# Kernel optimization log

Hardware: AMD Instinct MI355X
Metric: run time of the kernel (lower is better)

## Reference

```python
import jax, jax.numpy as jnp
import numpy as np

B, S, D, H = 2, 2048, 1024, 16  # batch, seq, rep_dim, num_heads
DH = D // H
MASK_VALUE = -1e-06  # value passed by MHAttention to masked_softmax (NOT -1e6)


def setup_inputs() -> dict:
    key = jax.random.key(0)
    ks = jax.random.split(key, 16)
    def xavier(k, shape):
        fan_in, fan_out = shape[0], shape[1]
        limit = float(np.sqrt(6.0 / (fan_in + fan_out)))
        return jax.random.uniform(k, shape, jnp.float32, -limit, limit)
    return {
        "queries": jax.random.normal(ks[0], (B, S, D), jnp.float32),
        "keys": jax.random.normal(ks[1], (B, S, D), jnp.float32),
        "values": jax.random.normal(ks[2], (B, S, D), jnp.float32),
        "thresholds": jax.random.randint(ks[3], (B,), 1, S + 1, jnp.int32),
        # Linear params stored as (in, out) so y = x @ W + b
        "Wq": xavier(ks[4], (D, D)), "bq": jnp.zeros((D,), jnp.float32),
        "Wk": xavier(ks[5], (D, D)), "bk": jnp.zeros((D,), jnp.float32),
        "Wv": xavier(ks[6], (D, D)), "bv": jnp.zeros((D,), jnp.float32),
        "W": xavier(ks[7], (DH, DH)),  # learnable bilinear attention matrix
        "Wo": xavier(ks[8], (D, D)), "bo": jnp.zeros((D,), jnp.float32),
    }


def reference(queries, keys, values, thresholds, Wq, bq, Wk, bk, Wv, bv, W, Wo, bo):
    def split_heads(x):  # (B,S,D) -> (B,H,S,DH)
        return x.reshape(B, S, H, DH).transpose(0, 2, 1, 3)

    Q = split_heads(queries @ Wq + bq)
    K = split_heads(keys @ Wk + bk)
    V = split_heads(values @ Wv + bv)

    # bilinear scores: (Q @ W) @ K^T, no 1/sqrt(d) scaling in original
    scores = jnp.einsum("bhqd,bhkd->bhqk", Q @ W, K)
    # mask key positions >= threshold[b] with MASK_VALUE before softmax
    keep = jnp.arange(S)[None, None, None, :] < thresholds[:, None, None, None]
    scores = jnp.where(keep, scores, MASK_VALUE)
    attn = jax.nn.softmax(scores, axis=-1)

    out = jnp.einsum("bhqk,bhkd->bhqd", attn, V)
    out = out.transpose(0, 2, 1, 3).reshape(B, S, D)  # merge heads
    return out @ Wo + bo
```

## Files before the change

### kernel.cpp

```cpp
#include <hip/hip_runtime.h>
#include <hip/hip_bf16.h>

#define D_MODEL 1024
#define NHEADS  16
#define DH      64
#define SEQ     2048
#define BATCH   2

#define LOG2E 1.4426950408889634f
#define MASKB2 (-1e-6f * LOG2E)
#define DEFER_THR 11.5456f
#define NEG_INF (-__builtin_inff())

typedef __attribute__((ext_vector_type(8))) short short8;
typedef __attribute__((ext_vector_type(4))) short short4v;
typedef __attribute__((ext_vector_type(4))) float f32x4;

#define AS1C(p) ((const __attribute__((address_space(1))) void*)(p))
#define AS3(p)  ((__attribute__((address_space(3))) void*)(p))

union PB { short4v s4; unsigned int u[2]; };

static __device__ __forceinline__ float fexp2(float x) {
    return __builtin_amdgcn_exp2f(x);
}

static __device__ __forceinline__ unsigned int pk2(float lo, float hi) {
    __hip_bfloat16 a = __float2bfloat16(lo), b = __float2bfloat16(hi);
    unsigned short au = *(unsigned short*)&a, bu = *(unsigned short*)&b;
    return (unsigned int)au | ((unsigned int)bu << 16);
}

__global__ __launch_bounds__(256) void fold_kernel(const float* __restrict__ Wq,
                                                   const float* __restrict__ bq,
                                                   const float* __restrict__ W,
                                                   float* __restrict__ Wq2,
                                                   float* __restrict__ bq2) {
    if (blockIdx.x < 4096) {
        int idx = blockIdx.x * 256 + threadIdx.x;
        int row = idx >> 10;
        int col = idx & 1023;
        int h = col >> 6, j = col & 63;
        const float* wqr = Wq + (size_t)row * D_MODEL + h * DH;
        float s = 0.f;
#pragma unroll
        for (int d = 0; d < DH; ++d) s += wqr[d] * W[d * DH + j];
        Wq2[idx] = s * LOG2E;
    } else {
        int col = (blockIdx.x - 4096) * 256 + threadIdx.x;
        int h = col >> 6, j = col & 63;
        float s = 0.f;
#pragma unroll
        for (int d = 0; d < DH; ++d) s += bq[h * DH + d] * W[d * DH + j];
        bq2[col] = s * LOG2E;
    }
}

__global__ __launch_bounds__(256) void convert3_kernel(const float* __restrict__ q,
                                                       const float* __restrict__ k,
                                                       const float* __restrict__ v,
                                                       __hip_bfloat16* __restrict__ oq,
                                                       __hip_bfloat16* __restrict__ ok,
                                                       __hip_bfloat16* __restrict__ ov) {
    int z = blockIdx.x >> 11;
    int i = (blockIdx.x & 2047) * 256 + threadIdx.x;
    const float* in = (z == 0) ? q : (z == 1) ? k : v;
    __hip_bfloat16* out = (z == 0) ? oq : (z == 1) ? ok : ov;
    float4 a = *(const float4*)(in + (size_t)i * 8);
    float4 b = *(const float4*)(in + (size_t)i * 8 + 4);
    __hip_bfloat16 o[8];
    o[0] = __float2bfloat16(a.x); o[1] = __float2bfloat16(a.y);
    o[2] = __float2bfloat16(a.z); o[3] = __float2bfloat16(a.w);
    o[4] = __float2bfloat16(b.x); o[5] = __float2bfloat16(b.y);
    o[6] = __float2bfloat16(b.z); o[7] = __float2bfloat16(b.w);
    *(short8*)(out + (size_t)i * 8) = *(short8*)o;
}

__global__ __launch_bounds__(256) void transpose4_kernel(const float* __restrict__ W0,
                                                         const float* __restrict__ W1,
                                                         const float* __restrict__ W2,
                                                         const float* __restrict__ W3,
                                                         __hip_bfloat16* __restrict__ T0,
                                                         __hip_bfloat16* __restrict__ T1,
                                                         __hip_bfloat16* __restrict__ T2,
                                                         __hip_bfloat16* __restrict__ T3) {
    __shared__ float sT[32][33];
    int z = blockIdx.z;
    const float* Win = (z == 0) ? W0 : (z == 1) ? W1 : (z == 2) ? W2 : W3;
    __hip_bfloat16* Wt = (z == 0) ? T0 : (z == 1) ? T1 : (z == 2) ? T2 : T3;
    int n0 = blockIdx.x * 32, k0 = blockIdx.y * 32;
    int tx = threadIdx.x & 31, ty = threadIdx.x >> 5;
#pragma unroll
    for (int i = 0; i < 4; ++i)
        sT[ty + i * 8][tx] = Win[(size_t)(k0 + ty + i * 8) * D_MODEL + n0 + tx];
    __syncthreads();
#pragma unroll
    for (int i = 0; i < 4; ++i)
        Wt[(size_t)(n0 + ty + i * 8) * D_MODEL + k0 + tx] = __float2bfloat16(sT[tx][ty + i * 8]);
}

#define GEMM_CORE(A_, BT_)                                                                  \
    __shared__ __hip_bfloat16 sA[2][128 * 32];                                              \
    __shared__ __hip_bfloat16 sB[2][64 * 32];                                               \
    const int t = threadIdx.x;                                                              \
    const int lane = t & 63, w = t >> 6;                                                    \
    const int g = lane >> 4, li = lane & 15;                                                \
    const int r0 = blockIdx.y * 128, c0 = blockIdx.x * 64;                                  \
    const int wr = (w >> 1) * 64, wc = (w & 1) * 32;                                        \
    f32x4 acc[4][2] = {};                                                                   \
    auto stage = [&](int bb, int k0) {                                                      \
        _Pragma("unroll")                                                                   \
        for (int i = 0; i < 2; ++i) {                                                       \
            int o = (i * 4 + w) * 1024 + lane * 16;                                         \
            int row = o >> 6, ce = (o & 63) >> 1;                                           \
            __builtin_amdgcn_global_load_lds(AS1C(A_ + (size_t)(r0 + row) * 1024 + k0 + ce),\
                                             AS3((char*)sA[bb] + (i * 4 + w) * 1024), 16, 0, 0); \
        }                                                                                   \
        {                                                                                   \
            int o = w * 1024 + lane * 16;                                                   \
            int row = o >> 6, ce = (o & 63) >> 1;                                           \
            __builtin_amdgcn_global_load_lds(AS1C(BT_ + (size_t)(c0 + row) * 1024 + k0 + ce),\
                                             AS3((char*)sB[bb] + w * 1024), 16, 0, 0);      \
        }                                                                                   \
    };                                                                                      \
    stage(0, 0);                                                                            \
    asm volatile("s_waitcnt vmcnt(0)" ::: "memory");                                        \
    __syncthreads();                                                                        \
    int cur = 0;                                                                            \
    for (int k0 = 0; k0 < 1024; k0 += 32) {                                                 \
        if (k0 + 32 < 1024) stage(cur ^ 1, k0 + 32);                                        \
        short8 af[4], bf[2];                                                                \
        _Pragma("unroll")                                                                   \
        for (int m = 0; m < 4; ++m)                                                         \
            af[m] = *(const short8*)(sA[cur] + (wr + m * 16 + li) * 32 + g * 8);            \
        _Pragma("unroll")                                                                   \
        for (int n = 0; n < 2; ++n)                                                         \
            bf[n] = *(const short8*)(sB[cur] + (wc + n * 16 + li) * 32 + g * 8);            \
        _Pragma("unroll")                                                                   \
        for (int m = 0; m < 4; ++m)                                                         \
            _Pragma("unroll")                                                               \
            for (int n = 0; n < 2; ++n)                                                     \
                acc[m][n] = __builtin_amdgcn_mfma_f32_16x16x32_bf16(af[m], bf[n], acc[m][n], 0, 0, 0); \
        asm volatile("s_waitcnt vmcnt(0)" ::: "memory");                                    \
        __syncthreads();                                                                    \
        cur ^= 1;                                                                           \
    }

__global__ __launch_bounds__(256) void gemm_qkv_kernel(
    const __hip_bfloat16* __restrict__ Xq, const __hip_bfloat16* __restrict__ Xk,
    const __hip_bfloat16* __restrict__ Xv,
    const __hip_bfloat16* __restrict__ WqT, const __hip_bfloat16* __restrict__ WkT,
    const __hip_bfloat16* __restrict__ WvT,
    const float* __restrict__ bq2, const float* __restrict__ bk, const float* __restrict__ bv,
    __hip_bfloat16* __restrict__ Qp, __hip_bfloat16* __restrict__ Kp,
    __hip_bfloat16* __restrict__ Vt) {
    const int z = blockIdx.z;
    const __hip_bfloat16* A  = (z == 0) ? Xq  : (z == 1) ? Xk  : Xv;
    const __hip_bfloat16* BT = (z == 0) ? WqT : (z == 1) ? WkT : WvT;
    const float* bias        = (z == 0) ? bq2 : (z == 1) ? bk  : bv;
    __hip_bfloat16* C        = (z == 0) ? Qp  : (z == 1) ? Kp  : Vt;

    GEMM_CORE(A, BT)

#pragma unroll
    for (int m = 0; m < 4; ++m) {
#pragma unroll
        for (int n = 0; n < 2; ++n) {
            int col = c0 + wc + n * 16 + li;
            float bs = bias[col];
            int row0 = r0 + wr + m * 16 + g * 4;
            int h = col >> 6, d = col & 63;
            if (z == 2) {
                int b = row0 >> 11, s0 = row0 & 2047;
                __hip_bfloat16 o4[4];
#pragma unroll
                for (int r = 0; r < 4; ++r) o4[r] = __float2bfloat16(acc[m][n][r] + bs);
                *(short4*)(C + (((size_t)(b * NHEADS + h)) * DH + d) * SEQ + s0) = *(short4*)o4;
            } else {
#pragma unroll
                for (int r = 0; r < 4; ++r) {
                    int row = row0 + r;
                    int b = row >> 11, s = row & 2047;
                    C[(((size_t)(b * NHEADS + h)) * SEQ + s) * DH + d] =
                        __float2bfloat16(acc[m][n][r] + bs);
                }
            }
        }
    }
}

__global__ __launch_bounds__(256) void gemm_out_kernel(
    const __hip_bfloat16* __restrict__ A, const __hip_bfloat16* __restrict__ BT,
    const float* __restrict__ bias, float* __restrict__ C) {
    GEMM_CORE(A, BT)
#pragma unroll
    for (int m = 0; m < 4; ++m) {
#pragma unroll
        for (int n = 0; n < 2; ++n) {
            int col = c0 + wc + n * 16 + li;
            float bs = bias[col];
            int row0 = r0 + wr + m * 16 + g * 4;
#pragma unroll
            for (int r = 0; r < 4; ++r)
                C[(size_t)(row0 + r) * D_MODEL + col] = acc[m][n][r] + bs;
        }
    }
}

__global__ __launch_bounds__(256) void vsum_kernel(const __hip_bfloat16* __restrict__ Vt,
                                                   const int* __restrict__ thresholds,
                                                   float* __restrict__ Vsum) {
    int bh = blockIdx.x, b = bh >> 4;
    int thresh = thresholds[b];
    int loop_end = min(SEQ, ((thresh + 63) >> 6) << 6);
    int t = threadIdx.x;
    int dh = t >> 2, sub = t & 3;
    const __hip_bfloat16* row = Vt + ((size_t)bh * DH + dh) * SEQ;
    float s = 0.f;
    for (int s0 = loop_end + sub * 8; s0 < SEQ; s0 += 32) {
        short8 v = *(const short8*)(row + s0);
#pragma unroll
        for (int j = 0; j < 8; ++j) {
            unsigned short us = (unsigned short)v[j];
            s += __bfloat162float(*(__hip_bfloat16*)&us);
        }
    }
    s += __shfl_xor(s, 1);
    s += __shfl_xor(s, 2);
    if (sub == 0) Vsum[bh * DH + dh] = s;
}

__global__ __launch_bounds__(256) void attn_mfma_kernel(
    const __hip_bfloat16* __restrict__ Qp,
    const __hip_bfloat16* __restrict__ Kp,
    const __hip_bfloat16* __restrict__ Vt,
    const int* __restrict__ thresholds,
    const float* __restrict__ Vsum,
    __hip_bfloat16* __restrict__ AO) {
    __shared__ char lds[32768];
    char* sK  = lds;
    char* sVT = lds + 16384;

    const int t = threadIdx.x, lane = t & 63, w = t >> 6;
    const int g = lane >> 4, li = lane & 15;
    const int bh = blockIdx.x, b = bh >> 4, h = bh & 15;
    const int q0 = blockIdx.y * 64;
    const int thresh = thresholds[b];
    const int loop_end = min(SEQ, ((thresh + 63) >> 6) << 6);
    const __hip_bfloat16* Qb = Qp + (size_t)bh * SEQ * DH;
    const __hip_bfloat16* Kb = Kp + (size_t)bh * SEQ * DH;
    const __hip_bfloat16* Vb = Vt + (size_t)bh * DH * SEQ;

    short8 qf[2];
#pragma unroll
    for (int kb = 0; kb < 2; ++kb)
        qf[kb] = *(const short8*)(Qb + (size_t)(q0 + w * 16 + li) * DH + kb * 32 + g * 8);

    f32x4 Oacc[4] = {};
    float mrun = NEG_INF, lrun = 0.f;

    auto stageK = [&](int bb, int kv) {
#pragma unroll
        for (int i = 0; i < 2; ++i) {
            int o = i * 4096 + w * 1024 + lane * 16;
            int key = o >> 7, slot = (o & 127) >> 4;
            __builtin_amdgcn_global_load_lds(
                AS1C(Kb + (size_t)(kv + key) * DH + ((slot ^ (key & 7)) << 3)),
                AS3(sK + bb * 8192 + i * 4096 + w * 1024), 16, 0, 0);
        }
    };
    auto stageV = [&](int bb, int kv) {
#pragma unroll
        for (int i = 0; i < 2; ++i) {
            int o = i * 4096 + w * 1024 + lane * 16;
            int dh = o >> 7, slot = (o & 127) >> 4;
            __builtin_amdgcn_global_load_lds(
                AS1C(Vb + (size_t)dh * SEQ + kv + ((slot ^ (dh & 7)) << 3)),
                AS3(sVT + bb * 8192 + i * 4096 + w * 1024), 16, 0, 0);
        }
    };

    stageK(0, 0); stageV(0, 0);
    asm volatile("s_waitcnt vmcnt(0)" ::: "memory");
    __syncthreads();

    int cur = 0;
    for (int kv0 = 0; kv0 < loop_end; kv0 += 64) {
        int nxt = kv0 + 64;
        if (nxt < loop_end) { stageK(cur ^ 1, nxt); stageV(cur ^ 1, nxt); }

        f32x4 S[4] = {};
        __builtin_amdgcn_s_setprio(1);
#pragma unroll
        for (int kb = 0; kb < 2; ++kb) {
            short8 kf[4];
#pragma unroll
            for (int n = 0; n < 4; ++n) {
                int key = 16 * n + li;
                kf[n] = *(const short8*)(sK + cur * 8192 + key * 128 +
                                         (((4 * kb + g) ^ (key & 7)) << 4));
            }
#pragma unroll
            for (int n = 0; n < 4; ++n)
                S[n] = __builtin_amdgcn_mfma_f32_16x16x32_bf16(kf[n], qf[kb], S[n], 0, 0, 0);
        }
        __builtin_amdgcn_s_setprio(0);

        if (kv0 + 64 > thresh) {
            int tr = thresh - kv0 - 4 * g;
#pragma unroll
            for (int n = 0; n < 4; ++n)
#pragma unroll
                for (int rr = 0; rr < 4; ++rr)
                    if (16 * n + rr >= tr) S[n][rr] = MASKB2;
        }

        float mx = S[0][0];
#pragma unroll
        for (int n = 0; n < 4; ++n)
#pragma unroll
            for (int rr = 0; rr < 4; ++rr) mx = fmaxf(mx, S[n][rr]);
        mx = fmaxf(mx, __shfl_xor(mx, 16));
        mx = fmaxf(mx, __shfl_xor(mx, 32));
        float pmax = mx;

        if (__any(pmax > mrun + DEFER_THR)) {
            float mn = fmaxf(mrun, pmax);
            float alpha = fexp2(mrun - mn);
            lrun *= alpha;
#pragma unroll
            for (int n = 0; n < 4; ++n)
#pragma unroll
                for (int rr = 0; rr < 4; ++rr) Oacc[n][rr] *= alpha;
            mrun = mn;
        }

        short4v pb[4];
        float rs = 0.f;
#pragma unroll
        for (int n = 0; n < 4; ++n) {
#pragma unroll
            for (int rr = 0; rr < 4; ++rr) {
                float p = fexp2(S[n][rr] - mrun);
                S[n][rr] = p;
                rs += p;
            }
            PB u;
            u.u[0] = pk2(S[n][0], S[n][1]);
            u.u[1] = pk2(S[n][2], S[n][3]);
            pb[n] = u.s4;
        }
        rs += __shfl_xor(rs, 16);
        rs += __shfl_xor(rs, 32);
        lrun += rs;

        __builtin_amdgcn_s_setprio(1);
#pragma unroll
        for (int ks = 0; ks < 4; ++ks) {
            int slot = 2 * ks + (g >> 1);
            int sub8 = 8 * (g & 1);
#pragma unroll
            for (int n = 0; n < 4; ++n) {
                int dh = 16 * n + li;
                short4v va = *(const short4v*)(sVT + cur * 8192 + dh * 128 +
                                               ((slot ^ (dh & 7)) << 4) + sub8);
                Oacc[n] = __builtin_amdgcn_mfma_f32_16x16x16bf16_1k(va, pb[ks], Oacc[n], 0, 0, 0);
            }
        }
        __builtin_amdgcn_s_setprio(0);

        asm volatile("s_waitcnt vmcnt(0)" ::: "memory");
        __syncthreads();
        cur ^= 1;
    }

    int nmask = SEQ - loop_end;
    if (nmask > 0) {
        const float* vs = Vsum + bh * DH;
        f32x4 vsf[4];
#pragma unroll
        for (int n = 0; n < 4; ++n) vsf[n] = *(const f32x4*)(vs + 16 * n + 4 * g);
        float pu = fexp2(MASKB2 - mrun);
        lrun += (float)nmask * pu;
#pragma unroll
        for (int n = 0; n < 4; ++n)
#pragma unroll
            for (int rr = 0; rr < 4; ++rr) Oacc[n][rr] += pu * vsf[n][rr];
    }

    float linv = 1.0f / lrun;
    int q = q0 + w * 16 + li;
#pragma unroll
    for (int n = 0; n < 4; ++n) {
        __hip_bfloat16 o4[4];
#pragma unroll
        for (int rr = 0; rr < 4; ++rr) o4[rr] = __float2bfloat16(Oacc[n][rr] * linv);
        *(short4*)(AO + (size_t)(b * SEQ + q) * D_MODEL + h * DH + 16 * n + 4 * g) =
            *(short4*)o4;
    }
}

extern "C" void kernel_launch(void* const* d_in, const int* in_sizes, int n_in,
                              void* d_out, int out_size, void* d_ws, size_t ws_size,
                              hipStream_t stream) {
    const float* queries    = (const float*)d_in[0];
    const float* keys       = (const float*)d_in[1];
    const float* values     = (const float*)d_in[2];
    const int*   thresholds = (const int*)d_in[3];
    const float* Wq = (const float*)d_in[4];
    const float* bq = (const float*)d_in[5];
    const float* Wk = (const float*)d_in[6];
    const float* bk = (const float*)d_in[7];
    const float* Wv = (const float*)d_in[8];
    const float* bv = (const float*)d_in[9];
    const float* W  = (const float*)d_in[10];
    const float* Wo = (const float*)d_in[11];
    const float* bo = (const float*)d_in[12];
    float* out = (float*)d_out;

    char* wsb = (char*)d_ws;
    float* bq2  = (float*)wsb;
    float* Vsum = (float*)(wsb + 4096);
    float* Wq2  = (float*)(wsb + 16384);
    __hip_bfloat16* XqB = (__hip_bfloat16*)(wsb + 16384 + (4 << 20));
    __hip_bfloat16* XkB = XqB + (1 << 22);
    __hip_bfloat16* XvB = XkB + (1 << 22);
    __hip_bfloat16* WqT = XvB + (1 << 22);
    __hip_bfloat16* WkT = WqT + (1 << 20);
    __hip_bfloat16* WvT = WkT + (1 << 20);
    __hip_bfloat16* WoT = WvT + (1 << 20);
    __hip_bfloat16* QpB = WoT + (1 << 20);
    __hip_bfloat16* KpB = QpB + (1 << 22);
    __hip_bfloat16* VtB = KpB + (1 << 22);
    __hip_bfloat16* AOB = XqB;

    fold_kernel<<<4100, 256, 0, stream>>>(Wq, bq, W, Wq2, bq2);
    convert3_kernel<<<6144, 256, 0, stream>>>(queries, keys, values, XqB, XkB, XvB);
    transpose4_kernel<<<dim3(32, 32, 4), 256, 0, stream>>>(Wq2, Wk, Wv, Wo,
                                                           WqT, WkT, WvT, WoT);

    gemm_qkv_kernel<<<dim3(16, 32, 3), 256, 0, stream>>>(XqB, XkB, XvB, WqT, WkT, WvT,
                                                         bq2, bk, bv, QpB, KpB, VtB);
    vsum_kernel<<<32, 256, 0, stream>>>(VtB, thresholds, Vsum);

    attn_mfma_kernel<<<dim3(32, 32), 256, 0, stream>>>(QpB, KpB, VtB, thresholds, Vsum, AOB);

    gemm_out_kernel<<<dim3(16, 32), 256, 0, stream>>>(AOB, WoT, bo, out);
}
```

Baseline: 179.2 us.

## Triple-buffer LDS staging in GEMM and attention loops with partial vmcnt waits

Turns the double-buffered global-to-LDS pipelines in the GEMM core and the attention kernel into triple-buffered ones that prefetch two tiles ahead. The per-iteration waits become partial vmcnt waits, so only the oldest tile's loads must land, and __syncthreads is replaced by a raw s_barrier. This is meant to hide more memory latency behind the MFMA work. In exchange LDS use grows (attention goes from 32KB to 48KB), which may reduce occupancy, and the vmcnt counts must match the number of outstanding loads exactly.

```diff
diff --git a/kernel.cpp b/kernel.cpp
--- a/kernel.cpp
+++ b/kernel.cpp
@@ -100,8 +100,8 @@
 }
 
 #define GEMM_CORE(A_, BT_)                                                                  \
-    __shared__ __hip_bfloat16 sA[2][128 * 32];                                              \
-    __shared__ __hip_bfloat16 sB[2][64 * 32];                                               \
+    __shared__ __hip_bfloat16 sA[3][128 * 32];                                              \
+    __shared__ __hip_bfloat16 sB[3][64 * 32];                                               \
     const int t = threadIdx.x;                                                              \
     const int lane = t & 63, w = t >> 6;                                                    \
     const int g = lane >> 4, li = lane & 15;                                                \
@@ -123,12 +123,15 @@
                                              AS3((char*)sB[bb] + w * 1024), 16, 0, 0);      \
         }                                                                                   \
     };                                                                                      \
-    stage(0, 0);                                                                            \
-    asm volatile("s_waitcnt vmcnt(0)" ::: "memory");                                        \
-    __syncthreads();                                                                        \
+    stage(0, 0); stage(1, 32);                                                              \
+    asm volatile("s_waitcnt vmcnt(3)" ::: "memory");                                        \
+    asm volatile("s_barrier" ::: "memory");                                                 \
     int cur = 0;                                                                            \
-    for (int k0 = 0; k0 < 1024; k0 += 32) {                                                 \
-        if (k0 + 32 < 1024) stage(cur ^ 1, k0 + 32);                                        \
+    for (int it = 0; it < 32; ++it) {                                                       \
+        if (it < 30) {                                                                      \
+            int nb = (cur + 2 >= 3) ? cur - 1 : cur + 2;                                    \
+            stage(nb, (it + 2) * 32);                                                       \
+        }                                                                                   \
         short8 af[4], bf[2];                                                                \
         _Pragma("unroll")                                                                   \
         for (int m = 0; m < 4; ++m)                                                         \
@@ -141,9 +144,12 @@
             _Pragma("unroll")                                                               \
             for (int n = 0; n < 2; ++n)                                                     \
                 acc[m][n] = __builtin_amdgcn_mfma_f32_16x16x32_bf16(af[m], bf[n], acc[m][n], 0, 0, 0); \
-        asm volatile("s_waitcnt vmcnt(0)" ::: "memory");                                    \
-        __syncthreads();                                                                    \
-        cur ^= 1;                                                                           \
+        if (it < 31) {                                                                      \
+            if (it < 30) asm volatile("s_waitcnt vmcnt(3)" ::: "memory");                   \
+            else         asm volatile("s_waitcnt vmcnt(0)" ::: "memory");                   \
+            asm volatile("s_barrier" ::: "memory");                                         \
+        }                                                                                   \
+        cur = (cur + 1 == 3) ? 0 : cur + 1;                                                 \
     }
 
 __global__ __launch_bounds__(256) void gemm_qkv_kernel(
@@ -237,9 +243,9 @@
     const int* __restrict__ thresholds,
     const float* __restrict__ Vsum,
     __hip_bfloat16* __restrict__ AO) {
-    __shared__ char lds[32768];
+    __shared__ char lds[49152];
     char* sK  = lds;
-    char* sVT = lds + 16384;
+    char* sVT = lds + 24576;
 
     const int t = threadIdx.x, lane = t & 63, w = t >> 6;
     const int g = lane >> 4, li = lane & 15;
@@ -247,6 +253,7 @@
     const int q0 = blockIdx.y * 64;
     const int thresh = thresholds[b];
     const int loop_end = min(SEQ, ((thresh + 63) >> 6) << 6);
+    const int nt = loop_end >> 6;
     const __hip_bfloat16* Qb = Qp + (size_t)bh * SEQ * DH;
     const __hip_bfloat16* Kb = Kp + (size_t)bh * SEQ * DH;
     const __hip_bfloat16* Vb = Vt + (size_t)bh * DH * SEQ;
@@ -281,13 +288,21 @@
     };
 
     stageK(0, 0); stageV(0, 0);
-    asm volatile("s_waitcnt vmcnt(0)" ::: "memory");
-    __syncthreads();
+    if (nt > 1) {
+        stageK(1, 64); stageV(1, 64);
+        asm volatile("s_waitcnt vmcnt(4)" ::: "memory");
+    } else {
+        asm volatile("s_waitcnt vmcnt(0)" ::: "memory");
+    }
+    asm volatile("s_barrier" ::: "memory");
 
     int cur = 0;
-    for (int kv0 = 0; kv0 < loop_end; kv0 += 64) {
-        int nxt = kv0 + 64;
-        if (nxt < loop_end) { stageK(cur ^ 1, nxt); stageV(cur ^ 1, nxt); }
+    for (int tt = 0; tt < nt; ++tt) {
+        const int kv0 = tt << 6;
+        if (tt + 2 < nt) {
+            int nb = (cur + 2 >= 3) ? cur - 1 : cur + 2;
+            stageK(nb, kv0 + 128); stageV(nb, kv0 + 128);
+        }
 
         f32x4 S[4] = {};
         __builtin_amdgcn_s_setprio(1);
@@ -369,9 +384,12 @@
         }
         __builtin_amdgcn_s_setprio(0);
 
-        asm volatile("s_waitcnt vmcnt(0)" ::: "memory");
-        __syncthreads();
-        cur ^= 1;
+        if (tt + 1 < nt) {
+            if (tt + 2 < nt) asm volatile("s_waitcnt vmcnt(4)" ::: "memory");
+            else             asm volatile("s_waitcnt vmcnt(0)" ::: "memory");
+            asm volatile("s_barrier" ::: "memory");
+        }
+        cur = (cur + 1 == 3) ? 0 : cur + 1;
     }
 
     int nmask = SEQ - loop_end;
```

Result: slower. 196.4 us (+9.6%).

## Process two query tiles per wave to reuse K/V LDS fragments

Applied to the files above, without the earlier changes.

Each wave now handles 32 query rows (two 16-row MFMA tiles) instead of 16, so each workgroup covers 128 queries and the grid halves. Every K and V fragment read from LDS feeds two MFMAs, which halves LDS traffic and global K/V staging per query. The cost is more registers for two sets of accumulators, softmax state and probabilities, possibly lower occupancy. The grid drops to 512 blocks, which may underfill the GPU's compute units.

```diff
diff --git a/kernel.cpp b/kernel.cpp
--- a/kernel.cpp
+++ b/kernel.cpp
@@ -244,20 +244,24 @@
     const int t = threadIdx.x, lane = t & 63, w = t >> 6;
     const int g = lane >> 4, li = lane & 15;
     const int bh = blockIdx.x, b = bh >> 4, h = bh & 15;
-    const int q0 = blockIdx.y * 64;
+    const int q0 = blockIdx.y * 128;
     const int thresh = thresholds[b];
     const int loop_end = min(SEQ, ((thresh + 63) >> 6) << 6);
     const __hip_bfloat16* Qb = Qp + (size_t)bh * SEQ * DH;
     const __hip_bfloat16* Kb = Kp + (size_t)bh * SEQ * DH;
     const __hip_bfloat16* Vb = Vt + (size_t)bh * DH * SEQ;
 
-    short8 qf[2];
-#pragma unroll
-    for (int kb = 0; kb < 2; ++kb)
-        qf[kb] = *(const short8*)(Qb + (size_t)(q0 + w * 16 + li) * DH + kb * 32 + g * 8);
-
-    f32x4 Oacc[4] = {};
-    float mrun = NEG_INF, lrun = 0.f;
+    short8 qf[2][2];
+#pragma unroll
+    for (int mq = 0; mq < 2; ++mq)
+#pragma unroll
+        for (int kb = 0; kb < 2; ++kb)
+            qf[mq][kb] = *(const short8*)(Qb + (size_t)(q0 + w * 32 + mq * 16 + li) * DH +
+                                          kb * 32 + g * 8);
+
+    f32x4 Oacc[2][4] = {};
+    float mrun[2] = {NEG_INF, NEG_INF};
+    float lrun[2] = {0.f, 0.f};
 
     auto stageK = [&](int bb, int kv) {
 #pragma unroll
@@ -289,7 +293,7 @@
         int nxt = kv0 + 64;
         if (nxt < loop_end) { stageK(cur ^ 1, nxt); stageV(cur ^ 1, nxt); }
 
-        f32x4 S[4] = {};
+        f32x4 S[2][4] = {};
         __builtin_amdgcn_s_setprio(1);
 #pragma unroll
         for (int kb = 0; kb < 2; ++kb) {
@@ -301,8 +305,11 @@
                                          (((4 * kb + g) ^ (key & 7)) << 4));
             }
 #pragma unroll
-            for (int n = 0; n < 4; ++n)
-                S[n] = __builtin_amdgcn_mfma_f32_16x16x32_bf16(kf[n], qf[kb], S[n], 0, 0, 0);
+            for (int mq = 0; mq < 2; ++mq)
+#pragma unroll
+                for (int n = 0; n < 4; ++n)
+                    S[mq][n] = __builtin_amdgcn_mfma_f32_16x16x32_bf16(kf[n], qf[mq][kb],
+                                                                       S[mq][n], 0, 0, 0);
         }
         __builtin_amdgcn_s_setprio(0);
 
@@ -312,47 +319,58 @@
             for (int n = 0; n < 4; ++n)
 #pragma unroll
                 for (int rr = 0; rr < 4; ++rr)
-                    if (16 * n + rr >= tr) S[n][rr] = MASKB2;
-        }
-
-        float mx = S[0][0];
-#pragma unroll
-        for (int n = 0; n < 4; ++n)
-#pragma unroll
-            for (int rr = 0; rr < 4; ++rr) mx = fmaxf(mx, S[n][rr]);
-        mx = fmaxf(mx, __shfl_xor(mx, 16));
-        mx = fmaxf(mx, __shfl_xor(mx, 32));
-        float pmax = mx;
-
-        if (__any(pmax > mrun + DEFER_THR)) {
-            float mn = fmaxf(mrun, pmax);
-            float alpha = fexp2(mrun - mn);
-            lrun *= alpha;
+                    if (16 * n + rr >= tr) { S[0][n][rr] = MASKB2; S[1][n][rr] = MASKB2; }
+        }
+
+        float pmax[2];
+#pragma unroll
+        for (int mq = 0; mq < 2; ++mq) {
+            float mx = S[mq][0][0];
 #pragma unroll
             for (int n = 0; n < 4; ++n)
 #pragma unroll
-                for (int rr = 0; rr < 4; ++rr) Oacc[n][rr] *= alpha;
-            mrun = mn;
-        }
-
-        short4v pb[4];
-        float rs = 0.f;
-#pragma unroll
-        for (int n = 0; n < 4; ++n) {
-#pragma unroll
-            for (int rr = 0; rr < 4; ++rr) {
-                float p = fexp2(S[n][rr] - mrun);
-                S[n][rr] = p;
-                rs += p;
+                for (int rr = 0; rr < 4; ++rr) mx = fmaxf(mx, S[mq][n][rr]);
+            mx = fmaxf(mx, __shfl_xor(mx, 16));
+            mx = fmaxf(mx, __shfl_xor(mx, 32));
+            pmax[mq] = mx;
+        }
+
+        bool need = (pmax[0] > mrun[0] + DEFER_THR) || (pmax[1] > mrun[1] + DEFER_THR);
+        if (__any(need)) {
+#pragma unroll
+            for (int mq = 0; mq < 2; ++mq) {
+                float mn = fmaxf(mrun[mq], pmax[mq]);
+                float alpha = fexp2(mrun[mq] - mn);
+                lrun[mq] *= alpha;
+#pragma unroll
+                for (int n = 0; n < 4; ++n)
+#pragma unroll
+                    for (int rr = 0; rr < 4; ++rr) Oacc[mq][n][rr] *= alpha;
+                mrun[mq] = mn;
             }
-            PB u;
-            u.u[0] = pk2(S[n][0], S[n][1]);
-            u.u[1] = pk2(S[n][2], S[n][3]);
-            pb[n] = u.s4;
-        }
-        rs += __shfl_xor(rs, 16);
-        rs += __shfl_xor(rs, 32);
-        lrun += rs;
+        }
+
+        short4v pb[2][4];
+#pragma unroll
+        for (int mq = 0; mq < 2; ++mq) {
+            float rs = 0.f;
+#pragma unroll
+            for (int n = 0; n < 4; ++n) {
+#pragma unroll
+                for (int rr = 0; rr < 4; ++rr) {
+                    float p = fexp2(S[mq][n][rr] - mrun[mq]);
+                    S[mq][n][rr] = p;
+                    rs += p;
+                }
+                PB u;
+                u.u[0] = pk2(S[mq][n][0], S[mq][n][1]);
+                u.u[1] = pk2(S[mq][n][2], S[mq][n][3]);
+                pb[mq][n] = u.s4;
+            }
+            rs += __shfl_xor(rs, 16);
+            rs += __shfl_xor(rs, 32);
+            lrun[mq] += rs;
+        }
 
         __builtin_amdgcn_s_setprio(1);
 #pragma unroll
@@ -364,7 +382,10 @@
                 int dh = 16 * n + li;
                 short4v va = *(const short4v*)(sVT + cur * 8192 + dh * 128 +
                                                ((slot ^ (dh & 7)) << 4) + sub8);
-                Oacc[n] = __builtin_amdgcn_mfma_f32_16x16x16bf16_1k(va, pb[ks], Oacc[n], 0, 0, 0);
+#pragma unroll
+                for (int mq = 0; mq < 2; ++mq)
+                    Oacc[mq][n] = __builtin_amdgcn_mfma_f32_16x16x16bf16_1k(va, pb[mq][ks],
+                                                                            Oacc[mq][n], 0, 0, 0);
             }
         }
         __builtin_amdgcn_s_setprio(0);
@@ -380,23 +401,29 @@
         f32x4 vsf[4];
 #pragma unroll
         for (int n = 0; n < 4; ++n) vsf[n] = *(const f32x4*)(vs + 16 * n + 4 * g);
-        float pu = fexp2(MASKB2 - mrun);
-        lrun += (float)nmask * pu;
-#pragma unroll
-        for (int n = 0; n < 4; ++n)
-#pragma unroll
-            for (int rr = 0; rr < 4; ++rr) Oacc[n][rr] += pu * vsf[n][rr];
-    }
-
-    float linv = 1.0f / lrun;
-    int q = q0 + w * 16 + li;
-#pragma unroll
-    for (int n = 0; n < 4; ++n) {
-        __hip_bfloat16 o4[4];
-#pragma unroll
-        for (int rr = 0; rr < 4; ++rr) o4[rr] = __float2bfloat16(Oacc[n][rr] * linv);
-        *(short4*)(AO + (size_t)(b * SEQ + q) * D_MODEL + h * DH + 16 * n + 4 * g) =
-            *(short4*)o4;
+#pragma unroll
+        for (int mq = 0; mq < 2; ++mq) {
+            float pu = fexp2(MASKB2 - mrun[mq]);
+            lrun[mq] += (float)nmask * pu;
+#pragma unroll
+            for (int n = 0; n < 4; ++n)
+#pragma unroll
+                for (int rr = 0; rr < 4; ++rr) Oacc[mq][n][rr] += pu * vsf[n][rr];
+        }
+    }
+
+#pragma unroll
+    for (int mq = 0; mq < 2; ++mq) {
+        float linv = 1.0f / lrun[mq];
+        int q = q0 + w * 32 + mq * 16 + li;
+#pragma unroll
+        for (int n = 0; n < 4; ++n) {
+            __hip_bfloat16 o4[4];
+#pragma unroll
+            for (int rr = 0; rr < 4; ++rr) o4[rr] = __float2bfloat16(Oacc[mq][n][rr] * linv);
+            *(short4*)(AO + (size_t)(b * SEQ + q) * D_MODEL + h * DH + 16 * n + 4 * g) =
+                *(short4*)o4;
+        }
     }
 }
 
@@ -443,7 +470,7 @@
                                                          bq2, bk, bv, QpB, KpB, VtB);
     vsum_kernel<<<32, 256, 0, stream>>>(VtB, thresholds, Vsum);
 
-    attn_mfma_kernel<<<dim3(32, 32), 256, 0, stream>>>(QpB, KpB, VtB, thresholds, Vsum, AOB);
+    attn_mfma_kernel<<<dim3(32, 16), 256, 0, stream>>>(QpB, KpB, VtB, thresholds, Vsum, AOB);
 
     gemm_out_kernel<<<dim3(16, 32), 256, 0, stream>>>(AOB, WoT, bo, out);
 }
```

New measurement: 181.6 us. No clear change (+1.3%).
